# Optimization experiments

Measured on AMD Instinct MI355X. Metric: run time of the kernel, lower is better.

## Reference

```python
import jax, jax.numpy as jnp
import numpy as np

B, L, D = 8, 4096, 512
H, DK = 8, 64           # num_heads, key_dim = D // H
SAMPLE_K = 512
CONV_K = 3
POOL = 2


def setup_inputs() -> dict:
    key = jax.random.key(0)
    ks = jax.random.split(key, 8)
    x = jax.random.normal(ks[0], (B, L, D), dtype=jnp.float32)
    sample_indices = jax.random.randint(ks[1], (SAMPLE_K,), 0, L, dtype=jnp.int32)
    s = 1.0 / np.sqrt(D)
    Wq = jax.random.uniform(ks[2], (D, H * DK), jnp.float32, -s, s)
    Wk = jax.random.uniform(ks[3], (D, H * DK), jnp.float32, -s, s)
    Wv = jax.random.uniform(ks[4], (D, H * DK), jnp.float32, -s, s)
    conv_w = jax.random.normal(ks[5], (CONV_K, H * DK, H * DK), jnp.float32) * 0.02
    conv_b = jnp.zeros((H * DK,), jnp.float32)
    comb_w = jax.random.normal(ks[6], (H * DK, D), jnp.float32) * 0.02
    comb_b = jnp.zeros((D,), jnp.float32)
    return {"x": x, "Wq": Wq, "Wk": Wk, "Wv": Wv, "conv_w": conv_w,
            "conv_b": conv_b, "comb_w": comb_w, "comb_b": comb_b,
            "sample_indices": sample_indices}


def reference(x, Wq, Wk, Wv, conv_w, conv_b, comb_w, comb_b, sample_indices):
    b, l, _ = x.shape
    # QKV projections -> [B, H, L, DK]
    Q = (x @ Wq).reshape(b, l, H, DK).transpose(0, 2, 1, 3)
    K = (x @ Wk).reshape(b, l, H, DK).transpose(0, 2, 1, 3)
    V = (x @ Wv).reshape(b, l, H, DK).transpose(0, 2, 1, 3)
    # sample K/V along sequence axis -> [B, H, S, DK]
    Ks = jnp.take(K, sample_indices, axis=2)
    Vs = jnp.take(V, sample_indices, axis=2)
    # scores [B, H, L, S]
    scores = jnp.einsum('bhld,bhsd->bhls', Q, Ks) / jnp.sqrt(jnp.float32(DK))
    # second gather along the sampled axis (size S); indices in [0, L) so
    # out-of-range indices are clipped (JAX default), matching jit-safe semantics
    scores = jnp.take(scores, sample_indices, axis=3, mode='clip')
    attn = jax.nn.softmax(scores, axis=-1)
    out = jnp.einsum('bhls,bhsd->bhld', attn, Vs)          # [B, H, L, DK]
    out = out.transpose(0, 2, 1, 3).reshape(b, l, H * DK)  # [B, L, E]
    # Conv1D, padding SAME, NWC / WIO
    out = jax.lax.conv_general_dilated(
        out, conv_w, window_strides=(1,), padding='SAME',
        dimension_numbers=('NWC', 'WIO', 'NWC')) + conv_b
    out = jax.nn.elu(out)
    # MaxPool1D: pool == stride, L divisible by POOL
    out = out.reshape(b, l // POOL, POOL, H * DK).max(axis=2)
    # combine heads (Dense back to D); Dropout is identity at inference
    out = out @ comb_w + comb_b
    return out
```

## Files before the change

### kernel.cpp

```cpp
#include <hip/hip_runtime.h>


typedef __attribute__((ext_vector_type(8))) short  short8;
typedef __attribute__((ext_vector_type(4))) short  short4b;
typedef __attribute__((ext_vector_type(4))) float  f32x4;

#define LSEQ   4096
#define SK     512
#define EDIM   512
#define LPAD   4098
#define PADROW 2098176

static __device__ __forceinline__ float bf2f(unsigned short h) {
    union { unsigned int u; float f; } v; v.u = ((unsigned int)h) << 16; return v.f;
}
static __device__ __forceinline__ unsigned short f2bf(float f) {
    union { float f; unsigned int u; } v; v.f = f;
    unsigned int r = (v.u + 0x7fffu + ((v.u >> 16) & 1u)) >> 16;
    return (unsigned short)r;
}

__global__ __launch_bounds__(256)
void cvt_bf16(const float* __restrict__ src, unsigned short* __restrict__ dst)
{
    const size_t i = ((size_t)blockIdx.x * 256 + threadIdx.x) * 8;
    const float4 a = *(const float4*)(src + i);
    const float4 b = *(const float4*)(src + i + 4);
    short8 o;
    o[0] = (short)f2bf(a.x); o[1] = (short)f2bf(a.y);
    o[2] = (short)f2bf(a.z); o[3] = (short)f2bf(a.w);
    o[4] = (short)f2bf(b.x); o[5] = (short)f2bf(b.y);
    o[6] = (short)f2bf(b.z); o[7] = (short)f2bf(b.w);
    *(short8*)(dst + i) = o;
}

__global__ __launch_bounds__(256)
void tr_f32_bf16(unsigned short* __restrict__ dst, const float* __restrict__ src,
                 int R, int C)
{
    __shared__ unsigned short T[64][72];
    const int t  = threadIdx.x;
    const int r0 = blockIdx.y * 64, c0 = blockIdx.x * 64;
    const int row = t >> 2, cg = (t & 3) * 16;
    const float* s = src + (size_t)(r0 + row) * C + c0 + cg;
    const float4 f0 = *(const float4*)s;
    const float4 f1 = *(const float4*)(s + 4);
    const float4 f2 = *(const float4*)(s + 8);
    const float4 f3 = *(const float4*)(s + 12);
    T[row][cg + 0]  = f2bf(f0.x); T[row][cg + 1]  = f2bf(f0.y);
    T[row][cg + 2]  = f2bf(f0.z); T[row][cg + 3]  = f2bf(f0.w);
    T[row][cg + 4]  = f2bf(f1.x); T[row][cg + 5]  = f2bf(f1.y);
    T[row][cg + 6]  = f2bf(f1.z); T[row][cg + 7]  = f2bf(f1.w);
    T[row][cg + 8]  = f2bf(f2.x); T[row][cg + 9]  = f2bf(f2.y);
    T[row][cg + 10] = f2bf(f2.z); T[row][cg + 11] = f2bf(f2.w);
    T[row][cg + 12] = f2bf(f3.x); T[row][cg + 13] = f2bf(f3.y);
    T[row][cg + 14] = f2bf(f3.z); T[row][cg + 15] = f2bf(f3.w);
    __syncthreads();
    unsigned short* d = dst + (size_t)(c0 + row) * R + r0 + cg;
    short8 o0, o1;
    #pragma unroll
    for (int k = 0; k < 8; ++k) o0[k] = (short)T[cg + k][row];
    #pragma unroll
    for (int k = 0; k < 8; ++k) o1[k] = (short)T[cg + 8 + k][row];
    *(short8*)d       = o0;
    *(short8*)(d + 8) = o1;
}

__global__ __launch_bounds__(256)
void tr_bf16(unsigned short* __restrict__ dst, const unsigned short* __restrict__ src,
             int R, int C)
{
    __shared__ unsigned short T[64][72];
    const size_t bofs = (size_t)blockIdx.z * (size_t)R * (size_t)C;
    src += bofs; dst += bofs;
    const int t  = threadIdx.x;
    const int r0 = blockIdx.y * 64, c0 = blockIdx.x * 64;
    const int row = t >> 2, cg = (t & 3) * 16;
    const unsigned short* s = src + (size_t)(r0 + row) * C + c0 + cg;
    *(short8*)&T[row][cg]     = *(const short8*)s;
    *(short8*)&T[row][cg + 8] = *(const short8*)(s + 8);
    __syncthreads();
    unsigned short* d = dst + (size_t)(c0 + row) * R + r0 + cg;
    short8 o0, o1;
    #pragma unroll
    for (int k = 0; k < 8; ++k) o0[k] = (short)T[cg + k][row];
    #pragma unroll
    for (int k = 0; k < 8; ++k) o1[k] = (short)T[cg + 8 + k][row];
    *(short8*)d       = o0;
    *(short8*)(d + 8) = o1;
}

__global__ __launch_bounds__(256)
void gather_rows(const unsigned short* __restrict__ xb, const int* __restrict__ sidx,
                 unsigned short* __restrict__ xkg, unsigned short* __restrict__ xvg)
{
    const int blk = blockIdx.x;
    const int b = blk >> 9, j = blk & 511;
    const int t = threadIdx.x;
    int qv = sidx[j];               qv = qv < 0 ? 0 : (qv > LSEQ - 1 ? LSEQ - 1 : qv);
    int cv = qv < SK - 1 ? qv : SK - 1;
    int pv = sidx[cv];              pv = pv < 0 ? 0 : (pv > LSEQ - 1 ? LSEQ - 1 : pv);
    const unsigned int* xs = (const unsigned int*)xb;
    unsigned int* kd = (unsigned int*)xkg;
    unsigned int* vd = (unsigned int*)xvg;
    const size_t dst = ((size_t)b * SK + j) * 256 + t;
    kd[dst] = xs[((size_t)b * LSEQ + pv) * 256 + t];
    vd[dst] = xs[((size_t)b * LSEQ + qv) * 256 + t];
}

__global__ __launch_bounds__(256)
void zero_pad(unsigned short* __restrict__ attpad)
{
    const int i = blockIdx.x * 256 + threadIdx.x;
    const int b = i >> 9, c = i & 511;
    attpad[(size_t)b * PADROW + c] = 0;
    attpad[(size_t)b * PADROW + (size_t)(LPAD - 1) * 512 + c] = 0;
}

template<int MODE>
__global__ __launch_bounds__(256)
void gemm128(const unsigned short* __restrict__ A, const unsigned short* __restrict__ Bt,
             const float* __restrict__ bias, void* __restrict__ Cout, int K)
{
    __shared__ unsigned short As[128 * 40];
    __shared__ unsigned short Bs[128 * 40];
    const int t    = threadIdx.x;
    const int n0   = blockIdx.x * 128;
    const int m0   = blockIdx.y * 128;
    const int srow = t >> 1, scg = (t & 1) * 16;
    const int lane = t & 63, wv = t >> 6;
    const int q = lane >> 4, ln = lane & 15;
    const int wm = (wv & 1) * 64, wn = (wv >> 1) * 64;

    const unsigned short* abase;
    if (MODE == 1) {
        const int gr = m0 + srow;
        abase = A + (size_t)(gr >> 12) * PADROW + (size_t)(gr & 4095) * 512;
    } else {
        abase = A + (size_t)(m0 + srow) * K;
    }
    const unsigned short* bbase = Bt + (size_t)(n0 + srow) * K;

    const f32x4 zero = {0.f, 0.f, 0.f, 0.f};
    f32x4 acc[4][4];
    #pragma unroll
    for (int i = 0; i < 4; ++i)
        #pragma unroll
        for (int j = 0; j < 4; ++j) acc[i][j] = zero;

    short8 av0 = *(const short8*)(abase + scg);
    short8 av1 = *(const short8*)(abase + scg + 8);
    short8 bv0 = *(const short8*)(bbase + scg);
    short8 bv1 = *(const short8*)(bbase + scg + 8);

    for (int k0 = 0; k0 < K; k0 += 32) {
        __syncthreads();
        *(short8*)&As[srow * 40 + scg]     = av0;
        *(short8*)&As[srow * 40 + scg + 8] = av1;
        *(short8*)&Bs[srow * 40 + scg]     = bv0;
        *(short8*)&Bs[srow * 40 + scg + 8] = bv1;
        __syncthreads();
        if (k0 + 32 < K) {
            av0 = *(const short8*)(abase + k0 + 32 + scg);
            av1 = *(const short8*)(abase + k0 + 32 + scg + 8);
            bv0 = *(const short8*)(bbase + k0 + 32 + scg);
            bv1 = *(const short8*)(bbase + k0 + 32 + scg + 8);
        }
        short8 af[4], bf[4];
        #pragma unroll
        for (int mt = 0; mt < 4; ++mt)
            af[mt] = *(const short8*)&As[(wm + mt * 16 + ln) * 40 + q * 8];
        #pragma unroll
        for (int nt = 0; nt < 4; ++nt)
            bf[nt] = *(const short8*)&Bs[(wn + nt * 16 + ln) * 40 + q * 8];
        #pragma unroll
        for (int mt = 0; mt < 4; ++mt)
            #pragma unroll
            for (int nt = 0; nt < 4; ++nt)
                acc[mt][nt] = __builtin_amdgcn_mfma_f32_16x16x32_bf16(af[mt], bf[nt], acc[mt][nt], 0, 0, 0);
    }

    if (MODE == 0) {
        unsigned short* C = (unsigned short*)Cout;
        #pragma unroll
        for (int mt = 0; mt < 4; ++mt)
            #pragma unroll
            for (int r = 0; r < 4; ++r) {
                const int grow = m0 + wm + mt * 16 + q * 4 + r;
                unsigned short* cp = C + (size_t)grow * 512 + n0 + wn + ln;
                #pragma unroll
                for (int nt = 0; nt < 4; ++nt) cp[nt * 16] = f2bf(acc[mt][nt][r]);
            }
    } else if (MODE == 2) {
        float* C = (float*)Cout;
        float bb[4];
        #pragma unroll
        for (int nt = 0; nt < 4; ++nt) bb[nt] = bias[n0 + wn + nt * 16 + ln];
        #pragma unroll
        for (int mt = 0; mt < 4; ++mt)
            #pragma unroll
            for (int r = 0; r < 4; ++r) {
                const int grow = m0 + wm + mt * 16 + q * 4 + r;
                float* cp = C + (size_t)grow * 512 + n0 + wn + ln;
                #pragma unroll
                for (int nt = 0; nt < 4; ++nt) cp[nt * 16] = acc[mt][nt][r] + bb[nt];
            }
    } else {
        unsigned short* C = (unsigned short*)Cout;
        float bb[4];
        #pragma unroll
        for (int nt = 0; nt < 4; ++nt) bb[nt] = bias[n0 + wn + nt * 16 + ln];
        #pragma unroll
        for (int mt = 0; mt < 4; ++mt) {
            const int grow = m0 + wm + mt * 16 + q * 4;
            const int b = grow >> 12, l = grow & 4095;
            unsigned short* cp = C + ((size_t)b * 2048 + (l >> 1)) * 512 + n0 + wn + ln;
            #pragma unroll
            for (int nt = 0; nt < 4; ++nt) {
                float v0 = acc[mt][nt][0] + bb[nt]; v0 = v0 > 0.f ? v0 : __expf(v0) - 1.f;
                float v1 = acc[mt][nt][1] + bb[nt]; v1 = v1 > 0.f ? v1 : __expf(v1) - 1.f;
                float v2 = acc[mt][nt][2] + bb[nt]; v2 = v2 > 0.f ? v2 : __expf(v2) - 1.f;
                float v3 = acc[mt][nt][3] + bb[nt]; v3 = v3 > 0.f ? v3 : __expf(v3) - 1.f;
                cp[nt * 16]       = f2bf(fmaxf(v0, v1));
                cp[512 + nt * 16] = f2bf(fmaxf(v2, v3));
            }
        }
    }
}

__global__ __launch_bounds__(256, 2)
void attn_fused(const unsigned short* __restrict__ xb, const unsigned short* __restrict__ WqT,
                const unsigned short* __restrict__ Kg, const unsigned short* __restrict__ Vt,
                unsigned short* __restrict__ attpad)
{
    __shared__ unsigned short Ks[128][72];
    __shared__ unsigned short Vs[64][136];
    __shared__ unsigned short Pp[128][136];
    const int t = threadIdx.x;
    const int wv = t >> 6, lane = t & 63, q = lane >> 4, ln = lane & 15;
    const int l0 = blockIdx.x * 128, h = blockIdx.y, b = blockIdx.z;
    const int qr0 = wv * 32;
    const f32x4 zero = {0.f, 0.f, 0.f, 0.f};

    const unsigned short* kgb = Kg + (size_t)b * SK * 512 + h * 64;
    const unsigned short* vtb = Vt + ((size_t)(b * EDIM + h * 64)) * SK;
    const int ksr = t >> 1, ksc = (t & 1) * 32;
    const int vsr = t >> 2, vsc = (t & 3) * 32;

    short8 kp0, kp1, kp2, kp3, vp0, vp1, vp2, vp3;
    {
        const unsigned short* ks = kgb + (size_t)ksr * 512 + ksc;
        kp0 = *(const short8*)ks;        kp1 = *(const short8*)(ks + 8);
        kp2 = *(const short8*)(ks + 16); kp3 = *(const short8*)(ks + 24);
        const unsigned short* vs = vtb + (size_t)vsr * SK + vsc;
        vp0 = *(const short8*)vs;        vp1 = *(const short8*)(vs + 8);
        vp2 = *(const short8*)(vs + 16); vp3 = *(const short8*)(vs + 24);
    }

    f32x4 qacc[2][4];
    #pragma unroll
    for (int g = 0; g < 2; ++g)
        #pragma unroll
        for (int nt = 0; nt < 4; ++nt) qacc[g][nt] = zero;
    const unsigned short* xr0 = xb + ((size_t)(b * LSEQ + l0 + qr0 + ln)) * 512 + q * 8;
    const unsigned short* xr1 = xr0 + (size_t)16 * 512;
    const unsigned short* wqp = WqT + ((size_t)(h * 64 + ln)) * 512 + q * 8;
    for (int ks = 0; ks < 16; ++ks) {
        const short8 ax0 = *(const short8*)(xr0 + ks * 32);
        const short8 ax1 = *(const short8*)(xr1 + ks * 32);
        #pragma unroll
        for (int nt = 0; nt < 4; ++nt) {
            const short8 bw = *(const short8*)(wqp + nt * 16 * 512 + ks * 32);
            qacc[0][nt] = __builtin_amdgcn_mfma_f32_16x16x32_bf16(ax0, bw, qacc[0][nt], 0, 0, 0);
            qacc[1][nt] = __builtin_amdgcn_mfma_f32_16x16x32_bf16(ax1, bw, qacc[1][nt], 0, 0, 0);
        }
    }
    #pragma unroll
    for (int g = 0; g < 2; ++g)
        #pragma unroll
        for (int nt = 0; nt < 4; ++nt)
            #pragma unroll
            for (int r = 0; r < 4; ++r)
                Pp[qr0 + g * 16 + q * 4 + r][nt * 16 + ln] = f2bf(qacc[g][nt][r]);
    asm volatile("s_waitcnt lgkmcnt(0)" ::: "memory");
    short8 bq[2][2];
    #pragma unroll
    for (int g = 0; g < 2; ++g) {
        bq[g][0] = *(const short8*)&Pp[qr0 + g * 16 + ln][q * 8];
        bq[g][1] = *(const short8*)&Pp[qr0 + g * 16 + ln][q * 8 + 32];
    }

    float m_run[2] = {-1e30f, -1e30f}, l_run[2] = {0.f, 0.f};
    f32x4 o[2][4];
    #pragma unroll
    for (int g = 0; g < 2; ++g)
        #pragma unroll
        for (int j = 0; j < 4; ++j) o[g][j] = zero;

    for (int c = 0; c < 4; ++c) {
        *(short8*)&Ks[ksr][ksc]      = kp0;  *(short8*)&Ks[ksr][ksc + 8]  = kp1;
        *(short8*)&Ks[ksr][ksc + 16] = kp2;  *(short8*)&Ks[ksr][ksc + 24] = kp3;
        *(short8*)&Vs[vsr][vsc]      = vp0;  *(short8*)&Vs[vsr][vsc + 8]  = vp1;
        *(short8*)&Vs[vsr][vsc + 16] = vp2;  *(short8*)&Vs[vsr][vsc + 24] = vp3;
        __syncthreads();

        f32x4 st[8][2];
        #pragma unroll
        for (int mt = 0; mt < 8; ++mt) {
            const short8 ak0 = *(const short8*)&Ks[mt * 16 + ln][q * 8];
            const short8 ak1 = *(const short8*)&Ks[mt * 16 + ln][q * 8 + 32];
            #pragma unroll
            for (int g = 0; g < 2; ++g) {
                f32x4 a = zero;
                a = __builtin_amdgcn_mfma_f32_16x16x32_bf16(ak0, bq[g][0], a, 0, 0, 0);
                a = __builtin_amdgcn_mfma_f32_16x16x32_bf16(ak1, bq[g][1], a, 0, 0, 0);
                #pragma unroll
                for (int r = 0; r < 4; ++r) a[r] *= 0.125f;
                st[mt][g] = a;
            }
        }

        float alpha_[2];
        #pragma unroll
        for (int g = 0; g < 2; ++g) {
            float mx = st[0][g][0];
            #pragma unroll
            for (int mt = 0; mt < 8; ++mt)
                #pragma unroll
                for (int r = 0; r < 4; ++r) mx = fmaxf(mx, st[mt][g][r]);
            mx = fmaxf(mx, __shfl_xor(mx, 16));
            mx = fmaxf(mx, __shfl_xor(mx, 32));
            const float m_new = fmaxf(m_run[g], mx);
            alpha_[g] = __expf(m_run[g] - m_new);
            m_run[g] = m_new;
            float ls = 0.f;
            #pragma unroll
            for (int mt = 0; mt < 8; ++mt) {
                short4b p4;
                #pragma unroll
                for (int r = 0; r < 4; ++r) {
                    const float p = __expf(st[mt][g][r] - m_new);
                    ls += p;
                    p4[r] = (short)f2bf(p);
                }
                *(short4b*)&Pp[qr0 + g * 16 + ln][mt * 16 + q * 4] = p4;
            }
            ls += __shfl_xor(ls, 16);
            ls += __shfl_xor(ls, 32);
            l_run[g] = l_run[g] * alpha_[g] + ls;
        }

        #pragma unroll
        for (int g = 0; g < 2; ++g) {
            #pragma unroll
            for (int r = 0; r < 4; ++r) {
                const float ab = __shfl(alpha_[g], q * 4 + r);
                #pragma unroll
                for (int j = 0; j < 4; ++j) o[g][j][r] *= ab;
            }
        }

        if (c < 3) {
            const unsigned short* ks = kgb + (size_t)((c + 1) * 128 + ksr) * 512 + ksc;
            kp0 = *(const short8*)ks;        kp1 = *(const short8*)(ks + 8);
            kp2 = *(const short8*)(ks + 16); kp3 = *(const short8*)(ks + 24);
            const unsigned short* vs = vtb + (size_t)vsr * SK + (c + 1) * 128 + vsc;
            vp0 = *(const short8*)vs;        vp1 = *(const short8*)(vs + 8);
            vp2 = *(const short8*)(vs + 16); vp3 = *(const short8*)(vs + 24);
        }

        asm volatile("s_waitcnt lgkmcnt(0)" ::: "memory");

        #pragma unroll
        for (int ks2 = 0; ks2 < 4; ++ks2) {
            const short8 ap0 = *(const short8*)&Pp[qr0 + ln][ks2 * 32 + q * 8];
            const short8 ap1 = *(const short8*)&Pp[qr0 + 16 + ln][ks2 * 32 + q * 8];
            #pragma unroll
            for (int j = 0; j < 4; ++j) {
                const short8 bv = *(const short8*)&Vs[j * 16 + ln][ks2 * 32 + q * 8];
                o[0][j] = __builtin_amdgcn_mfma_f32_16x16x32_bf16(ap0, bv, o[0][j], 0, 0, 0);
                o[1][j] = __builtin_amdgcn_mfma_f32_16x16x32_bf16(ap1, bv, o[1][j], 0, 0, 0);
            }
        }
        __syncthreads();
    }

    #pragma unroll
    for (int g = 0; g < 2; ++g) {
        const float li = 1.f / l_run[g];
        #pragma unroll
        for (int r = 0; r < 4; ++r) {
            const float ib = __shfl(li, q * 4 + r);
            const int rl = qr0 + g * 16 + q * 4 + r;
            #pragma unroll
            for (int j = 0; j < 4; ++j)
                attpad[((size_t)b * PADROW) + (size_t)(l0 + rl + 1) * 512 + h * 64 + j * 16 + ln]
                    = f2bf(o[g][j][r] * ib);
        }
    }
}

extern "C" void kernel_launch(void* const* d_in, const int* in_sizes, int n_in,
                              void* d_out, int out_size, void* d_ws, size_t ws_size,
                              hipStream_t stream)
{
    const float* x    = (const float*)d_in[0];
    const float* Wq   = (const float*)d_in[1];
    const float* Wk   = (const float*)d_in[2];
    const float* Wv   = (const float*)d_in[3];
    const float* cw   = (const float*)d_in[4];
    const float* cb   = (const float*)d_in[5];
    const float* mw   = (const float*)d_in[6];
    const float* mb2  = (const float*)d_in[7];
    const int*   sidx = (const int*)d_in[8];
    float* out = (float*)d_out;

    char* ws = (char*)d_ws;
    unsigned short* xb    = (unsigned short*)(ws + 0);
    unsigned short* Pool  = (unsigned short*)(ws + 0);
    unsigned short* Pad   = (unsigned short*)(ws + 33554432);
    unsigned short* xkg   = (unsigned short*)(ws + 33554432);
    unsigned short* xvg   = (unsigned short*)(ws + 37748736);
    unsigned short* Vg    = (unsigned short*)(ws + 41943040);
    unsigned short* Kg    = (unsigned short*)(ws + 67125248);
    unsigned short* Vt    = (unsigned short*)(ws + 71319552);
    unsigned short* WqT   = (unsigned short*)(ws + 75513856);
    unsigned short* WkT   = (unsigned short*)(ws + 76038144);
    unsigned short* WvT   = (unsigned short*)(ws + 76562432);
    unsigned short* CombT = (unsigned short*)(ws + 77086720);
    unsigned short* ConvT = (unsigned short*)(ws + 77611008);

    dim3 blk(256);

    cvt_bf16<<<dim3(8192), blk, 0, stream>>>(x, xb);

    tr_f32_bf16<<<dim3(8, 8),  blk, 0, stream>>>(WqT,   Wq, 512, 512);
    tr_f32_bf16<<<dim3(8, 8),  blk, 0, stream>>>(WkT,   Wk, 512, 512);
    tr_f32_bf16<<<dim3(8, 8),  blk, 0, stream>>>(WvT,   Wv, 512, 512);
    tr_f32_bf16<<<dim3(8, 8),  blk, 0, stream>>>(CombT, mw, 512, 512);
    tr_f32_bf16<<<dim3(8, 24), blk, 0, stream>>>(ConvT, cw, 1536, 512);

    gather_rows<<<dim3(4096), blk, 0, stream>>>(xb, sidx, xkg, xvg);

    gemm128<0><<<dim3(4, 32), blk, 0, stream>>>(xkg, WkT, nullptr, Kg, 512);
    gemm128<0><<<dim3(4, 32), blk, 0, stream>>>(xvg, WvT, nullptr, Vg, 512);

    tr_bf16<<<dim3(8, 8, 8), blk, 0, stream>>>(Vt, Vg, 512, 512);

    zero_pad<<<dim3(16), blk, 0, stream>>>(Pad);
    attn_fused<<<dim3(32, 8, 8), blk, 0, stream>>>(xb, WqT, Kg, Vt, Pad);

    gemm128<1><<<dim3(4, 256), blk, 0, stream>>>(Pad, ConvT, cb, Pool, 1536);

    gemm128<2><<<dim3(4, 128), blk, 0, stream>>>(Pool, CombT, mb2, out, 512);
}
```

Baseline: 387.2 us.

## Split softmax P tile into halves to shrink LDS and raise attention occupancy

The attention kernel now writes and consumes the bf16 probability tile in two 64-column halves instead of one 128-column tile. This halves the Pp shared buffer, cutting LDS per block enough that three blocks can fit per CU, and the launch bound is raised from 2 to 3 to match. Row-sum accumulation is deferred until after both halves, and the next K/V prefetch moves in between the halves. The tighter per-thread register budget under the higher occupancy target could cause spills, given the large score and accumulator arrays.

```diff
diff --git a/kernel.cpp b/kernel.cpp
--- a/kernel.cpp
+++ b/kernel.cpp
@@ -228,14 +228,14 @@
     }
 }
 
-__global__ __launch_bounds__(256, 2)
+__global__ __launch_bounds__(256, 3)
 void attn_fused(const unsigned short* __restrict__ xb, const unsigned short* __restrict__ WqT,
                 const unsigned short* __restrict__ Kg, const unsigned short* __restrict__ Vt,
                 unsigned short* __restrict__ attpad)
 {
     __shared__ unsigned short Ks[128][72];
     __shared__ unsigned short Vs[64][136];
-    __shared__ unsigned short Pp[128][136];
+    __shared__ unsigned short Pp[128][72];
     const int t = threadIdx.x;
     const int wv = t >> 6, lane = t & 63, q = lane >> 4, ln = lane & 15;
     const int l0 = blockIdx.x * 128, h = blockIdx.y, b = blockIdx.z;
@@ -320,7 +320,7 @@
             }
         }
 
-        float alpha_[2];
+        float alpha_[2], mcur[2], ls[2] = {0.f, 0.f};
         #pragma unroll
         for (int g = 0; g < 2; ++g) {
             float mx = st[0][g][0];
@@ -333,21 +333,7 @@
             const float m_new = fmaxf(m_run[g], mx);
             alpha_[g] = __expf(m_run[g] - m_new);
             m_run[g] = m_new;
-            float ls = 0.f;
-            #pragma unroll
-            for (int mt = 0; mt < 8; ++mt) {
-                short4b p4;
-                #pragma unroll
-                for (int r = 0; r < 4; ++r) {
-                    const float p = __expf(st[mt][g][r] - m_new);
-                    ls += p;
-                    p4[r] = (short)f2bf(p);
-                }
-                *(short4b*)&Pp[qr0 + g * 16 + ln][mt * 16 + q * 4] = p4;
-            }
-            ls += __shfl_xor(ls, 16);
-            ls += __shfl_xor(ls, 32);
-            l_run[g] = l_run[g] * alpha_[g] + ls;
+            mcur[g] = m_new;
         }
 
         #pragma unroll
@@ -360,27 +346,54 @@
             }
         }
 
-        if (c < 3) {
-            const unsigned short* ks = kgb + (size_t)((c + 1) * 128 + ksr) * 512 + ksc;
-            kp0 = *(const short8*)ks;        kp1 = *(const short8*)(ks + 8);
-            kp2 = *(const short8*)(ks + 16); kp3 = *(const short8*)(ks + 24);
-            const unsigned short* vs = vtb + (size_t)vsr * SK + (c + 1) * 128 + vsc;
-            vp0 = *(const short8*)vs;        vp1 = *(const short8*)(vs + 8);
-            vp2 = *(const short8*)(vs + 16); vp3 = *(const short8*)(vs + 24);
-        }
-
-        asm volatile("s_waitcnt lgkmcnt(0)" ::: "memory");
-
-        #pragma unroll
-        for (int ks2 = 0; ks2 < 4; ++ks2) {
-            const short8 ap0 = *(const short8*)&Pp[qr0 + ln][ks2 * 32 + q * 8];
-            const short8 ap1 = *(const short8*)&Pp[qr0 + 16 + ln][ks2 * 32 + q * 8];
-            #pragma unroll
-            for (int j = 0; j < 4; ++j) {
-                const short8 bv = *(const short8*)&Vs[j * 16 + ln][ks2 * 32 + q * 8];
-                o[0][j] = __builtin_amdgcn_mfma_f32_16x16x32_bf16(ap0, bv, o[0][j], 0, 0, 0);
-                o[1][j] = __builtin_amdgcn_mfma_f32_16x16x32_bf16(ap1, bv, o[1][j], 0, 0, 0);
-            }
+        #pragma unroll
+        for (int hh = 0; hh < 2; ++hh) {
+            #pragma unroll
+            for (int mtl = 0; mtl < 4; ++mtl) {
+                const int mt = hh * 4 + mtl;
+                #pragma unroll
+                for (int g = 0; g < 2; ++g) {
+                    short4b p4;
+                    #pragma unroll
+                    for (int r = 0; r < 4; ++r) {
+                        const float p = __expf(st[mt][g][r] - mcur[g]);
+                        ls[g] += p;
+                        p4[r] = (short)f2bf(p);
+                    }
+                    *(short4b*)&Pp[qr0 + g * 16 + ln][mtl * 16 + q * 4] = p4;
+                }
+            }
+
+            if (hh == 0 && c < 3) {
+                const unsigned short* ks = kgb + (size_t)((c + 1) * 128 + ksr) * 512 + ksc;
+                kp0 = *(const short8*)ks;        kp1 = *(const short8*)(ks + 8);
+                kp2 = *(const short8*)(ks + 16); kp3 = *(const short8*)(ks + 24);
+                const unsigned short* vs = vtb + (size_t)vsr * SK + (c + 1) * 128 + vsc;
+                vp0 = *(const short8*)vs;        vp1 = *(const short8*)(vs + 8);
+                vp2 = *(const short8*)(vs + 16); vp3 = *(const short8*)(vs + 24);
+            }
+
+            asm volatile("s_waitcnt lgkmcnt(0)" ::: "memory");
+
+            #pragma unroll
+            for (int ks2 = 0; ks2 < 2; ++ks2) {
+                const short8 ap0 = *(const short8*)&Pp[qr0 + ln][ks2 * 32 + q * 8];
+                const short8 ap1 = *(const short8*)&Pp[qr0 + 16 + ln][ks2 * 32 + q * 8];
+                #pragma unroll
+                for (int j = 0; j < 4; ++j) {
+                    const short8 bv = *(const short8*)&Vs[j * 16 + ln][(hh * 2 + ks2) * 32 + q * 8];
+                    o[0][j] = __builtin_amdgcn_mfma_f32_16x16x32_bf16(ap0, bv, o[0][j], 0, 0, 0);
+                    o[1][j] = __builtin_amdgcn_mfma_f32_16x16x32_bf16(ap1, bv, o[1][j], 0, 0, 0);
+                }
+            }
+        }
+
+        #pragma unroll
+        for (int g = 0; g < 2; ++g) {
+            float s2 = ls[g];
+            s2 += __shfl_xor(s2, 16);
+            s2 += __shfl_xor(s2, 32);
+            l_run[g] = l_run[g] * alpha_[g] + s2;
         }
         __syncthreads();
     }
```

Result: slower. 479.3 us (+23.8%).
